# Kernel tuning notes

Hardware: AMD Instinct MI355X
Metric: run time of the kernel (lower is better)

Reference implementation:

```python
import jax, jax.numpy as jnp
import numpy as np

H = 2048          # hidden_size
I = 768           # moe_intermediate_size
E = 64            # num_experts
TOP_K = 8         # num_experts_per_tok (norm_topk_prob=True)
B, S = 1, 1024


def setup_inputs() -> dict:
    key = jax.random.key(0)
    ks = jax.random.split(key, 5)
    scale = 0.02
    return {
        "hidden_states": jax.random.normal(ks[0], (B, S, H), dtype=jnp.float32),
        "W_router": jax.random.normal(ks[1], (H, E), dtype=jnp.float32) * scale,
        "W_gate": jax.random.normal(ks[2], (E, H, I), dtype=jnp.float32) * scale,
        "W_up": jax.random.normal(ks[3], (E, H, I), dtype=jnp.float32) * scale,
        "W_down": jax.random.normal(ks[4], (E, I, H), dtype=jnp.float32) * scale,
    }


def reference(hidden_states, W_router, W_gate, W_up, W_down):
    b, s, h = hidden_states.shape
    x = hidden_states.reshape(-1, h)                      # [T, H]

    # --- Qwen3MoeTopKRouter: linear gate -> fp32 softmax -> top-k -> renorm ---
    logits = x @ W_router                                 # [T, E]
    probs = jax.nn.softmax(logits.astype(jnp.float32), axis=-1)
    top_w, top_idx = jax.lax.top_k(probs, TOP_K)          # [T, K]
    top_w = top_w / jnp.sum(top_w, axis=-1, keepdims=True)  # norm_topk_prob
    top_w = top_w.astype(x.dtype)

    # combine weights per (token, expert): zero if expert not selected
    comb = jnp.sum(jax.nn.one_hot(top_idx, E, dtype=x.dtype) * top_w[..., None], axis=1)  # [T, E]

    # --- per-expert SwiGLU MLP: down(silu(gate(x)) * up(x)), dense-masked ---
    g = jnp.einsum('th,ehi->eti', x, W_gate)              # [E, T, I]
    u = jnp.einsum('th,ehi->eti', x, W_up)                # [E, T, I]
    hmid = jax.nn.silu(g) * u                             # [E, T, I]
    # fold combine weight into the intermediate to avoid an [E, T, H] buffer
    hmid = hmid * comb.T[:, :, None]                      # [E, T, I]
    out = jnp.einsum('eti,eih->th', hmid, W_down)         # [T, H]

    return out.reshape(b, s, h)
```

## Files before the change

kernel.cpp:

```cpp
#include <hip/hip_runtime.h>
#include <hip/hip_bf16.h>

#define H_DIM 2048
#define I_DIM 768
#define NEXP 64
#define TOPK 8
#define NTOK 1024
#define BM 256
#define BKS 32

typedef float f32x4 __attribute__((ext_vector_type(4)));
typedef float f32x2 __attribute__((ext_vector_type(2)));
typedef unsigned int u32x4 __attribute__((ext_vector_type(4)));
typedef unsigned int u32x2 __attribute__((ext_vector_type(2)));
typedef short bf16v8 __attribute__((ext_vector_type(8)));
typedef unsigned int u32;


__device__ inline unsigned short f2bf(float f) {
    union { float f; u32 u; } v; v.f = f;
    u32 r = (v.u + 0x7FFFu + ((v.u >> 16) & 1u)) >> 16;
    return (unsigned short)r;
}
__device__ inline u32 pack2(float a, float b) {
    return (u32)f2bf(a) | ((u32)f2bf(b) << 16);
}

__global__ void zero_kernel(float4* p, int n4) {
    int i = blockIdx.x * blockDim.x + threadIdx.x;
    if (i < n4) p[i] = (float4){0.f, 0.f, 0.f, 0.f};
}

__global__ void xconv_kernel(const float4* __restrict__ x, ushort4* __restrict__ xbf, int n4) {
    int i = blockIdx.x * blockDim.x + threadIdx.x;
    if (i < n4) {
        float4 v = x[i];
        ushort4 o;
        o.x = f2bf(v.x); o.y = f2bf(v.y); o.z = f2bf(v.z); o.w = f2bf(v.w);
        xbf[i] = o;
    }
}

__global__ __launch_bounds__(64) void router_kernel(
    const float* __restrict__ x, const float* __restrict__ Wr,
    int* __restrict__ topk_idx, float* __restrict__ topk_w)
{
    const int t = blockIdx.x;
    const int e = threadIdx.x;
    __shared__ float xs[H_DIM];

    const float* xrow = x + (size_t)t * H_DIM;
    #pragma unroll
    for (int m = 0; m < H_DIM / 64; ++m) xs[m * 64 + e] = xrow[m * 64 + e];
    __syncthreads();

    float acc = 0.f;
    #pragma unroll 8
    for (int h = 0; h < H_DIM; ++h) acc += xs[h] * Wr[(size_t)h * NEXP + e];

    float m = acc;
    #pragma unroll
    for (int o = 32; o > 0; o >>= 1) m = fmaxf(m, __shfl_xor(m, o));
    float p = __expf(acc - m);
    float s = p;
    #pragma unroll
    for (int o = 32; o > 0; o >>= 1) s += __shfl_xor(s, o);
    float prob = p / s;

    float myp = prob;
    float kw[TOPK]; int kid[TOPK]; float wsum = 0.f;
    #pragma unroll
    for (int k = 0; k < TOPK; ++k) {
        float v = myp; int bi = e;
        #pragma unroll
        for (int o = 32; o > 0; o >>= 1) {
            float ov = __shfl_xor(v, o);
            int   oi = __shfl_xor(bi, o);
            if (ov > v || (ov == v && oi < bi)) { v = ov; bi = oi; }
        }
        kw[k] = v; kid[k] = bi; wsum += v;
        if (e == bi) myp = -1.f;
    }
    if (e == 0) {
        float inv = 1.f / wsum;
        #pragma unroll
        for (int k = 0; k < TOPK; ++k) {
            topk_idx[t * TOPK + k] = kid[k];
            topk_w[t * TOPK + k]   = kw[k] * inv;
        }
    }
}

__global__ __launch_bounds__(64) void listbuild_kernel(
    const int* __restrict__ topk_idx, const float* __restrict__ topk_w,
    int* __restrict__ counts, int* __restrict__ lists, float* __restrict__ wlist)
{
    const int e = blockIdx.x;
    const int lane = threadIdx.x;
    int n = 0;
    for (int base = 0; base < NTOK * TOPK; base += 64) {
        int s = base + lane;
        int idx = topk_idx[s];
        bool match = (idx == e);
        unsigned long long mask = __ballot(match);
        int pre = __popcll(mask & ((1ull << lane) - 1ull));
        if (match) {
            lists[e * NTOK + n + pre] = s >> 3;
            wlist[e * NTOK + n + pre] = topk_w[s];
        }
        n += __popcll(mask);
    }
    if (lane == 0) counts[e] = n;
}

__global__ __launch_bounds__(64) void scan_kernel(
    const int* __restrict__ counts, int* __restrict__ offsets)
{
    int e = threadIdx.x;
    int v = counts[e];
    int xacc = v;
    #pragma unroll
    for (int o = 1; o < 64; o <<= 1) {
        int y = __shfl_up(xacc, o);
        if (e >= o) xacc += y;
    }
    offsets[e] = xacc - v;
}

__global__ __launch_bounds__(512) void gateup_kernel(
    const unsigned short* __restrict__ xbf,
    const float* __restrict__ Wg, const float* __restrict__ Wu,
    const int* __restrict__ counts, const int* __restrict__ offsets,
    const int* __restrict__ lists, const float* __restrict__ wlist,
    unsigned short* __restrict__ hmid)
{
    const int b  = blockIdx.x;
    const int wg = (b & 7) * 192 + (b >> 3);
    const int itile = wg % 24;
    const int e     = wg / 24;

    const int count = counts[e];
    if (count == 0) return;
    const int off = offsets[e];
    const int i0 = itile * 32;

    __shared__ unsigned short Alds[BM][40];
    __shared__ u32 Bgl[32 * 20];
    __shared__ u32 Bul[32 * 20];

    const int tid  = threadIdx.x;
    const int lane = tid & 63;
    const int wid  = tid >> 6;
    const int wm   = wid >> 1, wn = wid & 1;
    const int kb   = lane >> 4;
    const int l15  = lane & 15;

    const float* WgE = Wg + (size_t)e * H_DIM * I_DIM + i0;
    const float* WuE = Wu + (size_t)e * H_DIM * I_DIM + i0;

    const int ar = tid >> 1;
    const int ah = (tid & 1) * 16;
    const int bnn  = tid & 31;
    const int bkq  = (tid >> 5) & 7;
    const int bmat = tid >> 8;
    const float* WB = bmat ? WuE : WgE;
    const int key4w = 4 * ((bnn >> 3) & 3);
    u32* bdst = (bmat ? Bul : Bgl) + bnn * 20 + ((2 * bkq) ^ key4w);
    const int brn   = wn * 16 + l15;
    const int key4r = 4 * ((brn >> 3) & 3);

    for (int mstart = 0; mstart < count; mstart += BM) {
        const int pr = mstart + ar;
        const bool aact = pr < count;
        const unsigned short* xrow = xbf + (size_t)(aact ? lists[e * NTOK + pr] : 0) * H_DIM + ah;
        const bool mact = (mstart + wm * 64) < count;

        f32x4 accg[4], accu[4];
        #pragma unroll
        for (int i = 0; i < 4; ++i) {
            accg[i] = (f32x4){0.f, 0.f, 0.f, 0.f};
            accu[i] = (f32x4){0.f, 0.f, 0.f, 0.f};
        }

        u32x4 pA0, pA1;
        float b0a, b1a, b2a, b3a;
        float b0b, b1b, b2b, b3b;

#define LOADA(h)                                                                \
        if (aact) {                                                             \
            const u32x4* pa_ = (const u32x4*)(xrow + (h));                      \
            pA0 = pa_[0]; pA1 = pa_[1];                                         \
        }
#define LOADB(R0,R1,R2,R3,h)                                                    \
        {                                                                       \
            R0 = __builtin_nontemporal_load(WB + (size_t)((h) + 4 * bkq)     * I_DIM + bnn); \
            R1 = __builtin_nontemporal_load(WB + (size_t)((h) + 4 * bkq + 1) * I_DIM + bnn); \
            R2 = __builtin_nontemporal_load(WB + (size_t)((h) + 4 * bkq + 2) * I_DIM + bnn); \
            R3 = __builtin_nontemporal_load(WB + (size_t)((h) + 4 * bkq + 3) * I_DIM + bnn); \
        }
#define STOREA()                                                                \
        if (aact) {                                                             \
            *(u32x4*)&Alds[ar][ah]     = pA0;                                   \
            *(u32x4*)&Alds[ar][ah + 8] = pA1;                                   \
        }
#define STOREB(R0,R1,R2,R3)                                                     \
        {                                                                       \
            u32x2 w_; w_.x = pack2(R0, R1); w_.y = pack2(R2, R3);               \
            *(u32x2*)bdst = w_;                                                 \
        }
#define MFMA_PHASE()                                                            \
        if (mact) {                                                             \
            bf16v8 af[4], bg, bu;                                               \
            _Pragma("unroll")                                                   \
            for (int mf = 0; mf < 4; ++mf)                                      \
                af[mf] = *(const bf16v8*)&Alds[wm * 64 + mf * 16 + l15][kb * 8];\
            bg = *(const bf16v8*)&Bgl[brn * 20 + ((4 * kb) ^ key4r)];           \
            bu = *(const bf16v8*)&Bul[brn * 20 + ((4 * kb) ^ key4r)];           \
            _Pragma("unroll")                                                   \
            for (int mf = 0; mf < 4; ++mf) {                                    \
                accg[mf] = __builtin_amdgcn_mfma_f32_16x16x32_bf16(af[mf], bg, accg[mf], 0, 0, 0); \
                accu[mf] = __builtin_amdgcn_mfma_f32_16x16x32_bf16(af[mf], bu, accu[mf], 0, 0, 0); \
            }                                                                   \
        }

        LOADB(b0a, b1a, b2a, b3a, 0);
        LOADB(b0b, b1b, b2b, b3b, BKS);
        LOADA(0);

        for (int hh = 0; hh < H_DIM; hh += 2 * BKS) {
            STOREA(); STOREB(b0a, b1a, b2a, b3a);
            __syncthreads();
            if (hh + 2 * BKS < H_DIM) LOADB(b0a, b1a, b2a, b3a, hh + 2 * BKS);
            LOADA(hh + BKS);
            MFMA_PHASE();
            __syncthreads();

            STOREA(); STOREB(b0b, b1b, b2b, b3b);
            __syncthreads();
            if (hh + 3 * BKS < H_DIM) LOADB(b0b, b1b, b2b, b3b, hh + 3 * BKS);
            if (hh + 2 * BKS < H_DIM) LOADA(hh + 2 * BKS);
            MFMA_PHASE();
            __syncthreads();
        }
#undef LOADA
#undef LOADB
#undef STOREA
#undef STOREB
#undef MFMA_PHASE

        if (mact) {
            #pragma unroll
            for (int mf = 0; mf < 4; ++mf)
                #pragma unroll
                for (int r = 0; r < 4; ++r) {
                    int pos = mstart + wm * 64 + mf * 16 + kb * 4 + r;
                    if (pos < count) {
                        float wgt = wlist[e * NTOK + pos];
                        float g = accg[mf][r], u = accu[mf][r];
                        float s = 1.f / (1.f + __expf(-g));
                        float h = g * s * u * wgt;
                        hmid[(size_t)(off + pos) * I_DIM + i0 + wn * 16 + l15] = f2bf(h);
                    }
                }
        }
    }
}

__global__ __launch_bounds__(512) void down_kernel(
    const unsigned short* __restrict__ hmid, const float* __restrict__ Wd,
    const int* __restrict__ counts, const int* __restrict__ offsets,
    const int* __restrict__ lists, float* __restrict__ out)
{
    const int b  = blockIdx.x;
    const int wg = (b & 7) * 512 + (b >> 3);
    const int htile = wg % 64;
    const int e     = wg / 64;

    const int count = counts[e];
    if (count == 0) return;
    const int off = offsets[e];
    const int h0 = htile * 32;

    __shared__ unsigned short Alds[BM][40];
    __shared__ u32 Bdl[32 * 20];

    const int tid  = threadIdx.x;
    const int lane = tid & 63;
    const int wid  = tid >> 6;
    const int wm   = wid >> 1, wn = wid & 1;
    const int kb   = lane >> 4;
    const int l15  = lane & 15;

    const float* WdE = Wd + (size_t)e * I_DIM * H_DIM + h0;

    const int ar = tid >> 1;
    const int ah = (tid & 1) * 16;
    const int bnn  = tid & 31;
    const int bkq  = (tid >> 5) & 7;
    const bool bact = tid < 256;
    const int key4w = 4 * ((bnn >> 3) & 3);
    u32* bdst = Bdl + bnn * 20 + ((2 * bkq) ^ key4w);
    const int brn   = wn * 16 + l15;
    const int key4r = 4 * ((brn >> 3) & 3);

    for (int mstart = 0; mstart < count; mstart += BM) {
        const int pr = mstart + ar;
        const bool aact = pr < count;
        const unsigned short* hrow = hmid + (size_t)(off + (aact ? pr : 0)) * I_DIM + ah;
        const bool mact = (mstart + wm * 64) < count;

        f32x4 acc[4];
        #pragma unroll
        for (int i = 0; i < 4; ++i) acc[i] = (f32x4){0.f, 0.f, 0.f, 0.f};

        u32x4 pH0, pH1;
        float d0a, d1a, d2a, d3a;
        float d0b, d1b, d2b, d3b;

#define LOADA(k)                                                                \
        if (aact) {                                                             \
            const u32x4* p_ = (const u32x4*)(hrow + (k));                       \
            pH0 = p_[0]; pH1 = p_[1];                                           \
        }
#define LOADB(R0,R1,R2,R3,k)                                                    \
        if (bact) {                                                             \
            R0 = __builtin_nontemporal_load(WdE + (size_t)((k) + 4 * bkq)     * H_DIM + bnn); \
            R1 = __builtin_nontemporal_load(WdE + (size_t)((k) + 4 * bkq + 1) * H_DIM + bnn); \
            R2 = __builtin_nontemporal_load(WdE + (size_t)((k) + 4 * bkq + 2) * H_DIM + bnn); \
            R3 = __builtin_nontemporal_load(WdE + (size_t)((k) + 4 * bkq + 3) * H_DIM + bnn); \
        }
#define STOREA()                                                                \
        if (aact) {                                                             \
            *(u32x4*)&Alds[ar][ah]     = pH0;                                   \
            *(u32x4*)&Alds[ar][ah + 8] = pH1;                                   \
        }
#define STOREB(R0,R1,R2,R3)                                                     \
        if (bact) {                                                             \
            u32x2 w_; w_.x = pack2(R0, R1); w_.y = pack2(R2, R3);               \
            *(u32x2*)bdst = w_;                                                 \
        }
#define MFMA_PHASE()                                                            \
        if (mact) {                                                             \
            bf16v8 af[4], bd;                                                   \
            _Pragma("unroll")                                                   \
            for (int mf = 0; mf < 4; ++mf)                                      \
                af[mf] = *(const bf16v8*)&Alds[wm * 64 + mf * 16 + l15][kb * 8];\
            bd = *(const bf16v8*)&Bdl[brn * 20 + ((4 * kb) ^ key4r)];           \
            _Pragma("unroll")                                                   \
            for (int mf = 0; mf < 4; ++mf)                                      \
                acc[mf] = __builtin_amdgcn_mfma_f32_16x16x32_bf16(af[mf], bd, acc[mf], 0, 0, 0); \
        }

        LOADB(d0a, d1a, d2a, d3a, 0);
        LOADB(d0b, d1b, d2b, d3b, BKS);
        LOADA(0);

        for (int ii = 0; ii < I_DIM; ii += 2 * BKS) {
            STOREA(); STOREB(d0a, d1a, d2a, d3a);
            __syncthreads();
            if (ii + 2 * BKS < I_DIM) LOADB(d0a, d1a, d2a, d3a, ii + 2 * BKS);
            LOADA(ii + BKS);
            MFMA_PHASE();
            __syncthreads();

            STOREA(); STOREB(d0b, d1b, d2b, d3b);
            __syncthreads();
            if (ii + 3 * BKS < I_DIM) LOADB(d0b, d1b, d2b, d3b, ii + 3 * BKS);
            if (ii + 2 * BKS < I_DIM) LOADA(ii + 2 * BKS);
            MFMA_PHASE();
            __syncthreads();
        }
#undef LOADA
#undef LOADB
#undef STOREA
#undef STOREB
#undef MFMA_PHASE

        if (mact) {
            #pragma unroll
            for (int mf = 0; mf < 4; ++mf)
                #pragma unroll
                for (int r = 0; r < 4; ++r) {
                    int pos = mstart + wm * 64 + mf * 16 + kb * 4 + r;
                    if (pos < count) {
                        int tok = lists[e * NTOK + pos];
                        atomicAdd(&out[(size_t)tok * H_DIM + h0 + wn * 16 + l15],
                                  acc[mf][r]);
                    }
                }
        }
    }
}

extern "C" void kernel_launch(void* const* d_in, const int* in_sizes, int n_in,
                              void* d_out, int out_size, void* d_ws, size_t ws_size,
                              hipStream_t stream) {
    const float* x  = (const float*)d_in[0];
    const float* Wr = (const float*)d_in[1];
    const float* Wg = (const float*)d_in[2];
    const float* Wu = (const float*)d_in[3];
    const float* Wd = (const float*)d_in[4];
    float* out = (float*)d_out;

    char* ws = (char*)d_ws;
    int*   topk_idx = (int*)  (ws + 0);
    float* topk_w   = (float*)(ws + 32768);
    int*   counts   = (int*)  (ws + 65536);
    int*   offsets  = (int*)  (ws + 65792);
    int*   lists    = (int*)  (ws + 66048);
    float* wlist    = (float*)(ws + 328192);
    unsigned short* hmid = (unsigned short*)(ws + 590336);
    unsigned short* xbf  = (unsigned short*)(ws + 13173248);

    const int nout4 = NTOK * H_DIM / 4;
    hipLaunchKernelGGL(zero_kernel, dim3((nout4 + 255) / 256), dim3(256), 0, stream,
                       (float4*)out, nout4);
    hipLaunchKernelGGL(xconv_kernel, dim3((NTOK * H_DIM / 4 + 255) / 256), dim3(256), 0, stream,
                       (const float4*)x, (ushort4*)xbf, NTOK * H_DIM / 4);
    hipLaunchKernelGGL(router_kernel, dim3(NTOK), dim3(64), 0, stream,
                       x, Wr, topk_idx, topk_w);
    hipLaunchKernelGGL(listbuild_kernel, dim3(NEXP), dim3(64), 0, stream,
                       topk_idx, topk_w, counts, lists, wlist);
    hipLaunchKernelGGL(scan_kernel, dim3(1), dim3(64), 0, stream,
                       counts, offsets);
    hipLaunchKernelGGL(gateup_kernel, dim3(24 * NEXP), dim3(512), 0, stream,
                       xbf, Wg, Wu, counts, offsets, lists, wlist, hmid);
    hipLaunchKernelGGL(down_kernel, dim3(64 * NEXP), dim3(512), 0, stream,
                       hmid, Wd, counts, offsets, lists, out);
}
```

Measured before the change: 568.0 us.

## Replace down-projection atomics with bf16 partial buffer and per-token reduction

The down kernel can now write per-(expert, slot) partial outputs as bf16 into a workspace buffer instead of issuing fp32 atomicAdds into the output. A new reduce kernel sums each token's eight partials via an inverse map built during list construction, which also removes the output zeroing pass. The router is split across four waves that each reduce a quarter of the hidden dimension. The new path runs only when the workspace is large enough, costs extra memory traffic for the partial buffer, and rounds partials to bf16 before summation.

```diff
diff --git a/kernel.cpp b/kernel.cpp
--- a/kernel.cpp
+++ b/kernel.cpp
@@ -10,12 +10,15 @@
 #define BKS 32
 
 typedef float f32x4 __attribute__((ext_vector_type(4)));
-typedef float f32x2 __attribute__((ext_vector_type(2)));
 typedef unsigned int u32x4 __attribute__((ext_vector_type(4)));
 typedef unsigned int u32x2 __attribute__((ext_vector_type(2)));
 typedef short bf16v8 __attribute__((ext_vector_type(8)));
+typedef unsigned short u16x8 __attribute__((ext_vector_type(8)));
 typedef unsigned int u32;
 
+#define NTLOAD __builtin_nontemporal_load
+
+#define WS_NEEDED 50954752ull
 
 __device__ inline unsigned short f2bf(float f) {
     union { float f; u32 u; } v; v.f = f;
@@ -41,59 +44,75 @@
     }
 }
 
-__global__ __launch_bounds__(64) void router_kernel(
+__global__ __launch_bounds__(256) void router_kernel(
     const float* __restrict__ x, const float* __restrict__ Wr,
     int* __restrict__ topk_idx, float* __restrict__ topk_w)
 {
-    const int t = blockIdx.x;
-    const int e = threadIdx.x;
+    const int t   = blockIdx.x;
+    const int tid = threadIdx.x;
+    const int lane = tid & 63;
+    const int wv   = tid >> 6;
     __shared__ float xs[H_DIM];
+    __shared__ float red[4][64];
 
     const float* xrow = x + (size_t)t * H_DIM;
-    #pragma unroll
-    for (int m = 0; m < H_DIM / 64; ++m) xs[m * 64 + e] = xrow[m * 64 + e];
+    {
+        const float4* src = (const float4*)xrow;
+        float4* dst = (float4*)xs;
+        dst[tid]       = src[tid];
+        dst[tid + 256] = src[tid + 256];
+    }
     __syncthreads();
 
     float acc = 0.f;
+    const int h0 = wv * 512;
     #pragma unroll 8
-    for (int h = 0; h < H_DIM; ++h) acc += xs[h] * Wr[(size_t)h * NEXP + e];
-
-    float m = acc;
-    #pragma unroll
-    for (int o = 32; o > 0; o >>= 1) m = fmaxf(m, __shfl_xor(m, o));
-    float p = __expf(acc - m);
-    float s = p;
-    #pragma unroll
-    for (int o = 32; o > 0; o >>= 1) s += __shfl_xor(s, o);
-    float prob = p / s;
-
-    float myp = prob;
-    float kw[TOPK]; int kid[TOPK]; float wsum = 0.f;
-    #pragma unroll
-    for (int k = 0; k < TOPK; ++k) {
-        float v = myp; int bi = e;
-        #pragma unroll
-        for (int o = 32; o > 0; o >>= 1) {
-            float ov = __shfl_xor(v, o);
-            int   oi = __shfl_xor(bi, o);
-            if (ov > v || (ov == v && oi < bi)) { v = ov; bi = oi; }
-        }
-        kw[k] = v; kid[k] = bi; wsum += v;
-        if (e == bi) myp = -1.f;
-    }
-    if (e == 0) {
-        float inv = 1.f / wsum;
+    for (int h = h0; h < h0 + 512; ++h) acc += xs[h] * Wr[(size_t)h * NEXP + lane];
+    red[wv][lane] = acc;
+    __syncthreads();
+
+    if (tid < 64) {
+        const int e = tid;
+        float logit = red[0][e] + red[1][e] + red[2][e] + red[3][e];
+
+        float m = logit;
+        #pragma unroll
+        for (int o = 32; o > 0; o >>= 1) m = fmaxf(m, __shfl_xor(m, o));
+        float p = __expf(logit - m);
+        float s = p;
+        #pragma unroll
+        for (int o = 32; o > 0; o >>= 1) s += __shfl_xor(s, o);
+        float prob = p / s;
+
+        float myp = prob;
+        float kw[TOPK]; int kid[TOPK]; float wsum = 0.f;
         #pragma unroll
         for (int k = 0; k < TOPK; ++k) {
-            topk_idx[t * TOPK + k] = kid[k];
-            topk_w[t * TOPK + k]   = kw[k] * inv;
+            float v = myp; int bi = e;
+            #pragma unroll
+            for (int o = 32; o > 0; o >>= 1) {
+                float ov = __shfl_xor(v, o);
+                int   oi = __shfl_xor(bi, o);
+                if (ov > v || (ov == v && oi < bi)) { v = ov; bi = oi; }
+            }
+            kw[k] = v; kid[k] = bi; wsum += v;
+            if (e == bi) myp = -1.f;
+        }
+        if (e == 0) {
+            float inv = 1.f / wsum;
+            #pragma unroll
+            for (int k = 0; k < TOPK; ++k) {
+                topk_idx[t * TOPK + k] = kid[k];
+                topk_w[t * TOPK + k]   = kw[k] * inv;
+            }
         }
     }
 }
 
 __global__ __launch_bounds__(64) void listbuild_kernel(
     const int* __restrict__ topk_idx, const float* __restrict__ topk_w,
-    int* __restrict__ counts, int* __restrict__ lists, float* __restrict__ wlist)
+    int* __restrict__ counts, int* __restrict__ lists, float* __restrict__ wlist,
+    int* __restrict__ invmap)
 {
     const int e = blockIdx.x;
     const int lane = threadIdx.x;
@@ -107,6 +126,7 @@
         if (match) {
             lists[e * NTOK + n + pre] = s >> 3;
             wlist[e * NTOK + n + pre] = topk_w[s];
+            invmap[s] = n + pre;
         }
         n += __popcll(mask);
     }
@@ -127,6 +147,8 @@
     offsets[e] = xacc - v;
 }
 
+#define MFMA_BF16 __builtin_amdgcn_mfma_f32_16x16x32_bf16
+
 __global__ __launch_bounds__(512) void gateup_kernel(
     const unsigned short* __restrict__ xbf,
     const float* __restrict__ Wg, const float* __restrict__ Wu,
@@ -163,7 +185,7 @@
     const int bnn  = tid & 31;
     const int bkq  = (tid >> 5) & 7;
     const int bmat = tid >> 8;
-    const float* WB = bmat ? WuE : WgE;
+    const float* WB = (bmat ? Wu : Wg) + (size_t)e * H_DIM * I_DIM + i0 + bnn;
     const int key4w = 4 * ((bnn >> 3) & 3);
     u32* bdst = (bmat ? Bul : Bgl) + bnn * 20 + ((2 * bkq) ^ key4w);
     const int brn   = wn * 16 + l15;
@@ -186,29 +208,29 @@
         float b0a, b1a, b2a, b3a;
         float b0b, b1b, b2b, b3b;
 
-#define LOADA(h)                                                                \
+#define GU_LOADA(h)                                                             \
         if (aact) {                                                             \
             const u32x4* pa_ = (const u32x4*)(xrow + (h));                      \
             pA0 = pa_[0]; pA1 = pa_[1];                                         \
         }
-#define LOADB(R0,R1,R2,R3,h)                                                    \
+#define GU_LOADB(R0,R1,R2,R3,h)                                                 \
         {                                                                       \
-            R0 = __builtin_nontemporal_load(WB + (size_t)((h) + 4 * bkq)     * I_DIM + bnn); \
-            R1 = __builtin_nontemporal_load(WB + (size_t)((h) + 4 * bkq + 1) * I_DIM + bnn); \
-            R2 = __builtin_nontemporal_load(WB + (size_t)((h) + 4 * bkq + 2) * I_DIM + bnn); \
-            R3 = __builtin_nontemporal_load(WB + (size_t)((h) + 4 * bkq + 3) * I_DIM + bnn); \
-        }
-#define STOREA()                                                                \
+            R0 = NTLOAD(WB + (size_t)((h) + 4 * bkq)     * I_DIM);              \
+            R1 = NTLOAD(WB + (size_t)((h) + 4 * bkq + 1) * I_DIM);              \
+            R2 = NTLOAD(WB + (size_t)((h) + 4 * bkq + 2) * I_DIM);              \
+            R3 = NTLOAD(WB + (size_t)((h) + 4 * bkq + 3) * I_DIM);              \
+        }
+#define GU_STOREA()                                                             \
         if (aact) {                                                             \
             *(u32x4*)&Alds[ar][ah]     = pA0;                                   \
             *(u32x4*)&Alds[ar][ah + 8] = pA1;                                   \
         }
-#define STOREB(R0,R1,R2,R3)                                                     \
+#define GU_STOREB(R0,R1,R2,R3)                                                  \
         {                                                                       \
             u32x2 w_; w_.x = pack2(R0, R1); w_.y = pack2(R2, R3);               \
             *(u32x2*)bdst = w_;                                                 \
         }
-#define MFMA_PHASE()                                                            \
+#define GU_MFMA()                                                               \
         if (mact) {                                                             \
             bf16v8 af[4], bg, bu;                                               \
             _Pragma("unroll")                                                   \
@@ -218,35 +240,35 @@
             bu = *(const bf16v8*)&Bul[brn * 20 + ((4 * kb) ^ key4r)];           \
             _Pragma("unroll")                                                   \
             for (int mf = 0; mf < 4; ++mf) {                                    \
-                accg[mf] = __builtin_amdgcn_mfma_f32_16x16x32_bf16(af[mf], bg, accg[mf], 0, 0, 0); \
-                accu[mf] = __builtin_amdgcn_mfma_f32_16x16x32_bf16(af[mf], bu, accu[mf], 0, 0, 0); \
+                accg[mf] = MFMA_BF16(af[mf], bg, accg[mf], 0, 0, 0);            \
+                accu[mf] = MFMA_BF16(af[mf], bu, accu[mf], 0, 0, 0);            \
             }                                                                   \
         }
 
-        LOADB(b0a, b1a, b2a, b3a, 0);
-        LOADB(b0b, b1b, b2b, b3b, BKS);
-        LOADA(0);
+        GU_LOADB(b0a, b1a, b2a, b3a, 0);
+        GU_LOADB(b0b, b1b, b2b, b3b, BKS);
+        GU_LOADA(0);
 
         for (int hh = 0; hh < H_DIM; hh += 2 * BKS) {
-            STOREA(); STOREB(b0a, b1a, b2a, b3a);
-            __syncthreads();
-            if (hh + 2 * BKS < H_DIM) LOADB(b0a, b1a, b2a, b3a, hh + 2 * BKS);
-            LOADA(hh + BKS);
-            MFMA_PHASE();
-            __syncthreads();
-
-            STOREA(); STOREB(b0b, b1b, b2b, b3b);
-            __syncthreads();
-            if (hh + 3 * BKS < H_DIM) LOADB(b0b, b1b, b2b, b3b, hh + 3 * BKS);
-            if (hh + 2 * BKS < H_DIM) LOADA(hh + 2 * BKS);
-            MFMA_PHASE();
-            __syncthreads();
-        }
-#undef LOADA
-#undef LOADB
-#undef STOREA
-#undef STOREB
-#undef MFMA_PHASE
+            GU_STOREA(); GU_STOREB(b0a, b1a, b2a, b3a);
+            __syncthreads();
+            if (hh + 2 * BKS < H_DIM) GU_LOADB(b0a, b1a, b2a, b3a, hh + 2 * BKS);
+            GU_LOADA(hh + BKS);
+            GU_MFMA();
+            __syncthreads();
+
+            GU_STOREA(); GU_STOREB(b0b, b1b, b2b, b3b);
+            __syncthreads();
+            if (hh + 3 * BKS < H_DIM) GU_LOADB(b0b, b1b, b2b, b3b, hh + 3 * BKS);
+            if (hh + 2 * BKS < H_DIM) GU_LOADA(hh + 2 * BKS);
+            GU_MFMA();
+            __syncthreads();
+        }
+#undef GU_LOADA
+#undef GU_LOADB
+#undef GU_STOREA
+#undef GU_STOREB
+#undef GU_MFMA
 
         if (mact) {
             #pragma unroll
@@ -258,18 +280,19 @@
                         float wgt = wlist[e * NTOK + pos];
                         float g = accg[mf][r], u = accu[mf][r];
                         float s = 1.f / (1.f + __expf(-g));
-                        float h = g * s * u * wgt;
-                        hmid[(size_t)(off + pos) * I_DIM + i0 + wn * 16 + l15] = f2bf(h);
+                        hmid[(size_t)(off + pos) * I_DIM + i0 + wn * 16 + l15] = f2bf(g * s * u * wgt);
                     }
                 }
         }
     }
 }
 
+template <bool USE_PART>
 __global__ __launch_bounds__(512) void down_kernel(
     const unsigned short* __restrict__ hmid, const float* __restrict__ Wd,
     const int* __restrict__ counts, const int* __restrict__ offsets,
-    const int* __restrict__ lists, float* __restrict__ out)
+    const int* __restrict__ lists, float* __restrict__ out,
+    unsigned short* __restrict__ part)
 {
     const int b  = blockIdx.x;
     const int wg = (b & 7) * 512 + (b >> 3);
@@ -291,13 +314,12 @@
     const int kb   = lane >> 4;
     const int l15  = lane & 15;
 
-    const float* WdE = Wd + (size_t)e * I_DIM * H_DIM + h0;
-
     const int ar = tid >> 1;
     const int ah = (tid & 1) * 16;
     const int bnn  = tid & 31;
     const int bkq  = (tid >> 5) & 7;
     const bool bact = tid < 256;
+    const float* WB = Wd + (size_t)e * I_DIM * H_DIM + h0 + bnn;
     const int key4w = 4 * ((bnn >> 3) & 3);
     u32* bdst = Bdl + bnn * 20 + ((2 * bkq) ^ key4w);
     const int brn   = wn * 16 + l15;
@@ -317,29 +339,29 @@
         float d0a, d1a, d2a, d3a;
         float d0b, d1b, d2b, d3b;
 
-#define LOADA(k)                                                                \
+#define DN_LOADA(k)                                                             \
         if (aact) {                                                             \
             const u32x4* p_ = (const u32x4*)(hrow + (k));                       \
             pH0 = p_[0]; pH1 = p_[1];                                           \
         }
-#define LOADB(R0,R1,R2,R3,k)                                                    \
+#define DN_LOADB(R0,R1,R2,R3,k)                                                 \
         if (bact) {                                                             \
-            R0 = __builtin_nontemporal_load(WdE + (size_t)((k) + 4 * bkq)     * H_DIM + bnn); \
-            R1 = __builtin_nontemporal_load(WdE + (size_t)((k) + 4 * bkq + 1) * H_DIM + bnn); \
-            R2 = __builtin_nontemporal_load(WdE + (size_t)((k) + 4 * bkq + 2) * H_DIM + bnn); \
-            R3 = __builtin_nontemporal_load(WdE + (size_t)((k) + 4 * bkq + 3) * H_DIM + bnn); \
-        }
-#define STOREA()                                                                \
+            R0 = NTLOAD(WB + (size_t)((k) + 4 * bkq)     * H_DIM);              \
+            R1 = NTLOAD(WB + (size_t)((k) + 4 * bkq + 1) * H_DIM);              \
+            R2 = NTLOAD(WB + (size_t)((k) + 4 * bkq + 2) * H_DIM);              \
+            R3 = NTLOAD(WB + (size_t)((k) + 4 * bkq + 3) * H_DIM);              \
+        }
+#define DN_STOREA()                                                             \
         if (aact) {                                                             \
             *(u32x4*)&Alds[ar][ah]     = pH0;                                   \
             *(u32x4*)&Alds[ar][ah + 8] = pH1;                                   \
         }
-#define STOREB(R0,R1,R2,R3)                                                     \
+#define DN_STOREB(R0,R1,R2,R3)                                                  \
         if (bact) {                                                             \
             u32x2 w_; w_.x = pack2(R0, R1); w_.y = pack2(R2, R3);               \
             *(u32x2*)bdst = w_;                                                 \
         }
-#define MFMA_PHASE()                                                            \
+#define DN_MFMA()                                                               \
         if (mact) {                                                             \
             bf16v8 af[4], bd;                                                   \
             _Pragma("unroll")                                                   \
@@ -348,33 +370,33 @@
             bd = *(const bf16v8*)&Bdl[brn * 20 + ((4 * kb) ^ key4r)];           \
             _Pragma("unroll")                                                   \
             for (int mf = 0; mf < 4; ++mf)                                      \
-                acc[mf] = __builtin_amdgcn_mfma_f32_16x16x32_bf16(af[mf], bd, acc[mf], 0, 0, 0); \
-        }
-
-        LOADB(d0a, d1a, d2a, d3a, 0);
-        LOADB(d0b, d1b, d2b, d3b, BKS);
-        LOADA(0);
+                acc[mf] = MFMA_BF16(af[mf], bd, acc[mf], 0, 0, 0);              \
+        }
+
+        DN_LOADB(d0a, d1a, d2a, d3a, 0);
+        DN_LOADB(d0b, d1b, d2b, d3b, BKS);
+        DN_LOADA(0);
 
         for (int ii = 0; ii < I_DIM; ii += 2 * BKS) {
-            STOREA(); STOREB(d0a, d1a, d2a, d3a);
-            __syncthreads();
-            if (ii + 2 * BKS < I_DIM) LOADB(d0a, d1a, d2a, d3a, ii + 2 * BKS);
-            LOADA(ii + BKS);
-            MFMA_PHASE();
-            __syncthreads();
-
-            STOREA(); STOREB(d0b, d1b, d2b, d3b);
-            __syncthreads();
-            if (ii + 3 * BKS < I_DIM) LOADB(d0b, d1b, d2b, d3b, ii + 3 * BKS);
-            if (ii + 2 * BKS < I_DIM) LOADA(ii + 2 * BKS);
-            MFMA_PHASE();
-            __syncthreads();
-        }
-#undef LOADA
-#undef LOADB
-#undef STOREA
-#undef STOREB
-#undef MFMA_PHASE
+            DN_STOREA(); DN_STOREB(d0a, d1a, d2a, d3a);
+            __syncthreads();
+            if (ii + 2 * BKS < I_DIM) DN_LOADB(d0a, d1a, d2a, d3a, ii + 2 * BKS);
+            DN_LOADA(ii + BKS);
+            DN_MFMA();
+            __syncthreads();
+
+            DN_STOREA(); DN_STOREB(d0b, d1b, d2b, d3b);
+            __syncthreads();
+            if (ii + 3 * BKS < I_DIM) DN_LOADB(d0b, d1b, d2b, d3b, ii + 3 * BKS);
+            if (ii + 2 * BKS < I_DIM) DN_LOADA(ii + 2 * BKS);
+            DN_MFMA();
+            __syncthreads();
+        }
+#undef DN_LOADA
+#undef DN_LOADB
+#undef DN_STOREA
+#undef DN_STOREB
+#undef DN_MFMA
 
         if (mact) {
             #pragma unroll
@@ -383,13 +405,46 @@
                 for (int r = 0; r < 4; ++r) {
                     int pos = mstart + wm * 64 + mf * 16 + kb * 4 + r;
                     if (pos < count) {
-                        int tok = lists[e * NTOK + pos];
-                        atomicAdd(&out[(size_t)tok * H_DIM + h0 + wn * 16 + l15],
-                                  acc[mf][r]);
+                        if constexpr (USE_PART) {
+                            part[(size_t)(off + pos) * H_DIM + h0 + wn * 16 + l15] =
+                                f2bf(acc[mf][r]);
+                        } else {
+                            int tok = lists[e * NTOK + pos];
+                            atomicAdd(&out[(size_t)tok * H_DIM + h0 + wn * 16 + l15],
+                                      acc[mf][r]);
+                        }
                     }
                 }
         }
     }
+}
+
+__global__ __launch_bounds__(256) void reduce_kernel(
+    const unsigned short* __restrict__ part,
+    const int* __restrict__ topk_idx, const int* __restrict__ invmap,
+    const int* __restrict__ offsets, float* __restrict__ out)
+{
+    const int t   = blockIdx.x;
+    const int tid = threadIdx.x;
+    __shared__ int slots[TOPK];
+    if (tid < TOPK) {
+        int s = t * TOPK + tid;
+        slots[tid] = offsets[topk_idx[s]] + invmap[s];
+    }
+    __syncthreads();
+
+    const int c = tid * 8;
+    float acc[8] = {0.f, 0.f, 0.f, 0.f, 0.f, 0.f, 0.f, 0.f};
+    #pragma unroll
+    for (int k = 0; k < TOPK; ++k) {
+        u16x8 v = *(const u16x8*)&part[(size_t)slots[k] * H_DIM + c];
+        #pragma unroll
+        for (int j = 0; j < 8; ++j)
+            acc[j] += __uint_as_float((u32)(unsigned short)v[j] << 16);
+    }
+    float4* dst = (float4*)&out[(size_t)t * H_DIM + c];
+    dst[0] = (float4){acc[0], acc[1], acc[2], acc[3]};
+    dst[1] = (float4){acc[4], acc[5], acc[6], acc[7]};
 }
 
 extern "C" void kernel_launch(void* const* d_in, const int* in_sizes, int n_in,
@@ -409,22 +464,33 @@
     int*   offsets  = (int*)  (ws + 65792);
     int*   lists    = (int*)  (ws + 66048);
     float* wlist    = (float*)(ws + 328192);
-    unsigned short* hmid = (unsigned short*)(ws + 590336);
-    unsigned short* xbf  = (unsigned short*)(ws + 13173248);
-
-    const int nout4 = NTOK * H_DIM / 4;
-    hipLaunchKernelGGL(zero_kernel, dim3((nout4 + 255) / 256), dim3(256), 0, stream,
-                       (float4*)out, nout4);
+    int*   invmap   = (int*)  (ws + 590336);
+    unsigned short* hmid = (unsigned short*)(ws + 623104);
+    unsigned short* xbf  = (unsigned short*)(ws + 13206016);
+    unsigned short* part = (unsigned short*)(ws + 17400320);
+
+    const bool usePart = ws_size >= WS_NEEDED;
+
     hipLaunchKernelGGL(xconv_kernel, dim3((NTOK * H_DIM / 4 + 255) / 256), dim3(256), 0, stream,
                        (const float4*)x, (ushort4*)xbf, NTOK * H_DIM / 4);
-    hipLaunchKernelGGL(router_kernel, dim3(NTOK), dim3(64), 0, stream,
+    hipLaunchKernelGGL(router_kernel, dim3(NTOK), dim3(256), 0, stream,
                        x, Wr, topk_idx, topk_w);
     hipLaunchKernelGGL(listbuild_kernel, dim3(NEXP), dim3(64), 0, stream,
-                       topk_idx, topk_w, counts, lists, wlist);
+                       topk_idx, topk_w, counts, lists, wlist, invmap);
     hipLaunchKernelGGL(scan_kernel, dim3(1), dim3(64), 0, stream,
                        counts, offsets);
     hipLaunchKernelGGL(gateup_kernel, dim3(24 * NEXP), dim3(512), 0, stream,
                        xbf, Wg, Wu, counts, offsets, lists, wlist, hmid);
-    hipLaunchKernelGGL(down_kernel, dim3(64 * NEXP), dim3(512), 0, stream,
-                       hmid, Wd, counts, offsets, lists, out);
-}
+    if (usePart) {
+        hipLaunchKernelGGL((down_kernel<true>), dim3(64 * NEXP), dim3(512), 0, stream,
+                           hmid, Wd, counts, offsets, lists, out, part);
+        hipLaunchKernelGGL(reduce_kernel, dim3(NTOK), dim3(256), 0, stream,
+                           part, topk_idx, invmap, offsets, out);
+    } else {
+        const int nout4 = NTOK * H_DIM / 4;
+        hipLaunchKernelGGL(zero_kernel, dim3((nout4 + 255) / 256), dim3(256), 0, stream,
+                           (float4*)out, nout4);
+        hipLaunchKernelGGL((down_kernel<false>), dim3(64 * NEXP), dim3(512), 0, stream,
+                           hmid, Wd, counts, offsets, lists, out, part);
+    }
+}
```

Measured after the change: 489.2 us. 1.16x faster.
